# Optimization experiments

Hardware: AMD Instinct MI355X
Metric: run time of the kernel (lower is better)

## Reference

```python
import jax, jax.numpy as jnp
import numpy as np

DG = 8   # deformable groups
K = 9    # 3x3 kernel taps


def _conv3x3(x, w, b):
    y = jax.lax.conv_general_dilated(x, w, (1, 1), ((1, 1), (1, 1)),
                                     dimension_numbers=('NCHW', 'OIHW', 'NCHW'))
    return y + b[None, :, None, None]


def _deform_conv_v2(x, off_y, off_x, mask, w, b):
    # x: [B,C,H,W], off_*/mask: [B,DG,K,H,W], w: [Cout,C,3,3], b: [Cout]
    B, C, H, W = x.shape
    cpg = C // DG
    k = jnp.arange(K)
    ky = (k // 3 - 1).astype(x.dtype)[None, None, :, None, None]
    kx = (k % 3 - 1).astype(x.dtype)[None, None, :, None, None]
    hh = jnp.arange(H, dtype=x.dtype)[None, None, None, :, None]
    ww = jnp.arange(W, dtype=x.dtype)[None, None, None, None, :]
    py = hh + ky + off_y            # sampling rows  [B,DG,K,H,W]
    px = ww + kx + off_x            # sampling cols
    y0 = jnp.floor(py); x0 = jnp.floor(px)
    ly = py - y0; lx = px - x0
    xf = x.reshape(B, DG, cpg, H * W)

    def corner(yi, xi):
        valid = ((yi >= 0) & (yi < H) & (xi >= 0) & (xi < W)).astype(x.dtype)
        idx = (jnp.clip(yi, 0, H - 1) * W + jnp.clip(xi, 0, W - 1)).astype(jnp.int32)
        idxb = jnp.broadcast_to(idx.reshape(B, DG, 1, K * H * W), (B, DG, cpg, K * H * W))
        v = jnp.take_along_axis(xf, idxb, axis=3).reshape(B, DG, cpg, K, H, W)
        return v, valid

    v00, m00 = corner(y0, x0)
    v01, m01 = corner(y0, x0 + 1)
    v10, m10 = corner(y0 + 1, x0)
    v11, m11 = corner(y0 + 1, x0 + 1)
    w00 = ((1 - ly) * (1 - lx) * m00)[:, :, None]
    w01 = ((1 - ly) * lx * m01)[:, :, None]
    w10 = (ly * (1 - lx) * m10)[:, :, None]
    w11 = (ly * lx * m11)[:, :, None]
    val = (v00 * w00 + v01 * w01 + v10 * w10 + v11 * w11) * mask[:, :, None]
    wr = w.reshape(w.shape[0], DG, cpg, K)
    return jnp.einsum('bgckhw,ogck->bohw', val, wr) + b[None, :, None, None]


def reference(feat_l, feat_s, w_atten, w_fsm, w_off, w_cm, b_cm, w_dcn, b_dcn):
    B, C, H, W = feat_l.shape
    # bilinear upsample (align_corners=False == half-pixel centers, matches jax.image.resize)
    feat_up = jax.image.resize(feat_s, (B, feat_s.shape[1], H, W), method='bilinear')
    # FeatureSelectionModule: SE-style gate + residual + 1x1 proj
    gap = feat_l.mean(axis=(2, 3))                       # [B,C]
    atten = jax.nn.sigmoid(gap @ w_atten.T)[:, :, None, None]
    xg = feat_l * (1.0 + atten)                          # x + x*atten
    feat_arm = jnp.einsum('bchw,oc->bohw', xg, w_fsm)
    # offset feature: 1x1 conv over cat([feat_arm, 2*feat_up])
    cat = jnp.concatenate([feat_arm, feat_up * 2.0], axis=1)
    off_feat = jnp.einsum('bchw,oc->bohw', cat, w_off)
    # dcn_v2 internal conv_offset_mask -> o1, o2, mask
    om = _conv3x3(off_feat, w_cm, b_cm)                  # [B, DG*3*K, H, W]
    n = DG * K
    off_y = om[:, :n].reshape(B, DG, K, H, W)
    off_x = om[:, n:2 * n].reshape(B, DG, K, H, W)
    mask = jax.nn.sigmoid(om[:, 2 * n:]).reshape(B, DG, K, H, W)
    out = _deform_conv_v2(feat_up, off_y, off_x, mask, w_dcn, b_dcn)
    return jax.nn.relu(out) + feat_arm


def setup_inputs() -> dict:
    key = jax.random.key(0)
    ks = jax.random.split(key, 9)
    B, C, H, W = 8, 128, 64, 64
    return {
        'feat_l': jax.random.normal(ks[0], (B, C, H, W), jnp.float32),
        'feat_s': jax.random.normal(ks[1], (B, C, H // 2, W // 2), jnp.float32),
        'w_atten': jax.random.normal(ks[2], (C, C), jnp.float32) / np.sqrt(C),
        'w_fsm': jax.random.normal(ks[3], (C, C), jnp.float32) / np.sqrt(C),
        'w_off': jax.random.normal(ks[4], (C, 2 * C), jnp.float32) / np.sqrt(2 * C),
        'w_cm': jax.random.normal(ks[5], (DG * 3 * K, C, 3, 3), jnp.float32) * 0.01,
        'b_cm': jnp.zeros((DG * 3 * K,), jnp.float32),
        'w_dcn': jax.random.normal(ks[6], (C, C, 3, 3), jnp.float32) / np.sqrt(C * 9),
        'b_dcn': jax.random.normal(ks[7], (C,), jnp.float32) * 0.01,
    }
```

## Files before the change

kernel.cpp:

```cpp
#include <hip/hip_runtime.h>
#include <hip/hip_bf16.h>

constexpr int Bn = 8, Cn = 128, Hn = 64, Wn = 64, HWn = Hn * Wn;
constexpr int DGn = 8, Kn = 9, CMn = 216;
constexpr int Hs = 32, Ws = 32, HWs = Hs * Ws;

typedef __attribute__((ext_vector_type(8))) short bf16x8;
typedef __attribute__((ext_vector_type(4))) float f32x4;

constexpr long OFF_FLAG = 0;
constexpr long OFF_FLB  = 256;
constexpr long OFF_FUPB = OFF_FLB  + (long)Bn*HWn*Cn/2;
constexpr long OFF_OFT  = OFF_FUPB + (long)Bn*HWn*Cn/2;
constexpr long OFF_WCT  = OFF_OFT  + (long)Bn*HWn*Cn/2;
constexpr long OFF_WDT  = OFF_WCT  + (long)18*224*64/2 + 64;
constexpr long OFF_P    = OFF_WDT  + (long)Kn*Cn*Cn/2 + 64;
constexpr long OFF_W1TB = OFF_P    + 16384;
constexpr long OFF_WCAT = OFF_W1TB + (long)Bn*Cn*Cn/2;
constexpr long OFF_BCM  = OFF_WCAT + (long)Bn*Cn*256/2;
constexpr long OFF_BDC  = OFF_BCM + 256;
constexpr long OFF_GAP  = OFF_BDC + 256;
constexpr long OFF_AT   = OFF_GAP + 1024;
constexpr long OFF_FARM = OFF_AT  + 1024;
constexpr long OFF_OM   = OFF_FARM + (long)Bn*Cn*HWn;

static __device__ __forceinline__ float ldin(const void* p, long i, bool isbf) {
  if (isbf) return __bfloat162float(((const __hip_bfloat16*)p)[i]);
  return ((const float*)p)[i];
}
static __device__ __forceinline__ unsigned short f2b(float f) {
  unsigned u = __builtin_bit_cast(unsigned, f);
  u += 0x7FFFu + ((u >> 16) & 1u);
  return (unsigned short)(u >> 16);
}
static __device__ __forceinline__ unsigned pack2(float v0, float v1) {
  return ((unsigned)f2b(v1) << 16) | (unsigned)f2b(v0);
}
static __device__ __forceinline__ float b2f(unsigned short s) {
  return __builtin_bit_cast(float, ((unsigned)s) << 16);
}

#define GLOAD_LDS16(g, l) __builtin_amdgcn_global_load_lds( \
    (const __attribute__((address_space(1))) void*)(g),     \
    (__attribute__((address_space(3))) void*)(l), 16, 0, 0)

__global__ __launch_bounds__(256) void k_detect(const unsigned int* __restrict__ p,
                                                int* __restrict__ flag,
                                                float* __restrict__ gap) {
  __shared__ int cnt[256];
  int t = threadIdx.x;
  int c = 0;
  for (int i = 0; i < 4; ++i) {
    unsigned v = p[t * 4 + i];
    unsigned e = (v >> 7) & 0xFFu;
    c += (e >= 118u && e <= 130u) ? 1 : 0;
  }
  cnt[t] = c;
#pragma unroll
  for (int i = 0; i < 4; ++i) gap[t + i * 256] = 0.f;
  __syncthreads();
  for (int s = 128; s > 0; s >>= 1) {
    if (t < s) cnt[t] += cnt[t + s];
    __syncthreads();
  }
  if (t == 0) *flag = (cnt[0] > 512) ? 1 : 0;
}

__global__ __launch_bounds__(256) void k_prep(const void* __restrict__ b_cm,
                                              const void* __restrict__ b_dcn,
                                              const void* __restrict__ w_cm,
                                              const void* __restrict__ w_dcn,
                                              const void* __restrict__ woff,
                                              const void* __restrict__ wfsm,
                                              float* __restrict__ bcm_d,
                                              float* __restrict__ bdc_d,
                                              unsigned short* __restrict__ wcb,
                                              unsigned short* __restrict__ wdb,
                                              float* __restrict__ P,
                                              const int* __restrict__ flag) {
  const int bid = blockIdx.x, t = threadIdx.x;
  const bool isbf = (*flag != 0);
  if (bid == 0) {
    if (t < CMn) bcm_d[t] = ldin(b_cm, t, isbf);
    if (t < Cn)  bdc_d[t] = ldin(b_dcn, t, isbf);
    return;
  }
  if (bid < 1 + 1008) {
    int i = (bid - 1) * 256 + t;
    if (i >= 18 * 224 * 64) return;
    int s = i / (224 * 64);
    int rem = i % (224 * 64);
    int oc = rem >> 6, c_off = rem & 63;
    int tap = s >> 1, ck = s & 1;
    int c = ck * 64 + c_off;
    float v = 0.f;
    if (oc < CMn) v = ldin(w_cm, ((long)oc * Cn + c) * Kn + tap, isbf);
    int chunk = c_off >> 3, e = c_off & 7;
    int pc = chunk ^ (oc & 7);
    wcb[(long)s * 14336 + oc * 64 + pc * 8 + e] = f2b(v);
    return;
  }
  if (bid < 1 + 1008 + 576) {
    int i = (bid - 1 - 1008) * 256 + t;
    if (i >= Kn * Cn * Cn) return;
    int e = i & 7, lh = (i >> 3) & 3, o = (i >> 5) & 127;
    int ks = (i >> 12) & 3, k = i >> 14;
    int c = ks * 32 + lh * 8 + e;
    wdb[i] = f2b(ldin(w_dcn, ((long)o * Cn + c) * Kn + k, isbf));
    return;
  }
  {
    int idx = (bid - 1 - 1008 - 576) * 256 + t;
    if (idx >= Cn * Cn) return;
    int o = idx >> 7, k = idx & 127;
    float s = 0.f;
    for (int c = 0; c < Cn; ++c)
      s += ldin(woff, (long)o * 256 + c, isbf) * ldin(wfsm, (long)c * Cn + k, isbf);
    P[idx] = s;
  }
}

__global__ __launch_bounds__(256) void k_cvtlup(const void* __restrict__ feat_l,
                                                const void* __restrict__ fs,
                                                unsigned short* __restrict__ flb,
                                                unsigned short* __restrict__ fupb,
                                                float* __restrict__ gap,
                                                const int* __restrict__ flag) {
  __shared__ float sh[8448];
  const int b = blockIdx.y, t = threadIdx.x;
  const bool isbf = (*flag != 0);
  if (blockIdx.z == 0) {
    const int p0 = blockIdx.x * 64;
    for (int i = t; i < 8192; i += 256) {
      int c = i >> 6, p = i & 63;
      sh[c * 65 + p] = ldin(feat_l, (long)(b * Cn + c) * HWn + p0 + p, isbf);
    }
    __syncthreads();
    if (t < 128) {
      float s = 0.f;
#pragma unroll
      for (int p = 0; p < 64; ++p) s += sh[t * 65 + p];
      atomicAdd(&gap[b * Cn + t], s * (1.0f / HWn));
    }
    for (int i = t; i < 1024; i += 256) {
      int p = i >> 4, ch = (i & 15) * 8;
      uint4 pk;
      pk.x = pack2(sh[(ch + 0) * 65 + p], sh[(ch + 1) * 65 + p]);
      pk.y = pack2(sh[(ch + 2) * 65 + p], sh[(ch + 3) * 65 + p]);
      pk.z = pack2(sh[(ch + 4) * 65 + p], sh[(ch + 5) * 65 + p]);
      pk.w = pack2(sh[(ch + 6) * 65 + p], sh[(ch + 7) * 65 + p]);
      *(uint4*)(flb + (((long)(b * HWn + p0 + p)) << 7) + ch) = pk;
    }
  } else {
    const int h = blockIdx.x;
    int iy0; float fy;
    if (h & 1) { iy0 = (h - 1) >> 1; fy = 0.25f; } else { iy0 = (h >> 1) - 1; fy = 0.75f; }
    int iy1 = min(iy0 + 1, Hs - 1); iy0 = max(iy0, 0);
    for (int i = t; i < 8192; i += 256) {
      int sel = i >> 12, c = (i >> 5) & 127, x = i & 31;
      int iy = sel ? iy1 : iy0;
      sh[sel * 4224 + c * 33 + x] = ldin(fs, (long)(b * Cn + c) * HWs + iy * Ws + x, isbf);
    }
    __syncthreads();
    for (int i = t; i < 1024; i += 256) {
      int w = i >> 4, ch0 = (i & 15) * 8;
      int ix0; float fx;
      if (w & 1) { ix0 = (w - 1) >> 1; fx = 0.25f; } else { ix0 = (w >> 1) - 1; fx = 0.75f; }
      int ix1 = min(ix0 + 1, Ws - 1); ix0 = max(ix0, 0);
      float v[8];
#pragma unroll
      for (int j = 0; j < 8; ++j) {
        int c = ch0 + j;
        v[j] = (1.f - fy) * ((1.f - fx) * sh[c * 33 + ix0] + fx * sh[c * 33 + ix1]) +
               fy         * ((1.f - fx) * sh[4224 + c * 33 + ix0] + fx * sh[4224 + c * 33 + ix1]);
      }
      uint4 pk;
      pk.x = pack2(v[0], v[1]); pk.y = pack2(v[2], v[3]);
      pk.z = pack2(v[4], v[5]); pk.w = pack2(v[6], v[7]);
      *(uint4*)(fupb + (((long)(b * HWn + h * Wn + w)) << 7) + ch0) = pk;
    }
  }
}

__global__ __launch_bounds__(256) void k_atten(const float* __restrict__ gap,
                                               const void* __restrict__ wat,
                                               float* __restrict__ at1p,
                                               const int* __restrict__ flag) {
  int tid = blockIdx.x * 256 + threadIdx.x;
  if (tid >= Bn * Cn) return;
  int b = tid >> 7, o = tid & 127;
  bool isbf = (*flag != 0);
  const float* g = gap + b * Cn;
  float s = 0.f;
  for (int c = 0; c < Cn; ++c) s += g[c] * ldin(wat, (long)o * Cn + c, isbf);
  at1p[tid] = 1.0f + 1.0f / (1.0f + expf(-s));
}

__global__ __launch_bounds__(256) void k_wprep(const void* __restrict__ wfsm,
                                               const void* __restrict__ woff,
                                               const float* __restrict__ P,
                                               const float* __restrict__ at1p,
                                               unsigned short* __restrict__ w1tb,
                                               unsigned short* __restrict__ wcat,
                                               const int* __restrict__ flag) {
  int idx = blockIdx.x * 256 + threadIdx.x;
  if (idx >= Bn * 49152) return;
  bool isbf = (*flag != 0);
  int b = idx / 49152, r = idx % 49152;
  if (r < 16384) {
    int o = r >> 7, k = r & 127;
    w1tb[((long)(b * Cn + o) << 7) + k] =
        f2b(ldin(wfsm, (long)o * Cn + k, isbf) * at1p[b * Cn + k]);
  } else {
    r -= 16384;
    int o = r >> 8, k = r & 255;
    float v = (k < 128) ? P[o * Cn + k] * at1p[b * Cn + k]
                        : 2.0f * ldin(woff, (long)o * 256 + k, isbf);
    wcat[((long)(b * Cn + o) << 8) + k] = f2b(v);
  }
}

__global__ __launch_bounds__(256) void k_fao(const unsigned short* __restrict__ flb,
                                             const unsigned short* __restrict__ fupb,
                                             const unsigned short* __restrict__ w1tb,
                                             const unsigned short* __restrict__ wcat,
                                             float* __restrict__ farm,
                                             unsigned short* __restrict__ oftb) {
  const int b = blockIdx.y, m0 = blockIdx.x * 32;
  const int t = threadIdx.x, lane = t & 63, wv = t >> 6;
  const int lm = lane & 15, lh = lane >> 4;
  f32x4 accF[2][2], accO[2][2];
#pragma unroll
  for (int mt = 0; mt < 2; ++mt)
#pragma unroll
    for (int nt = 0; nt < 2; ++nt) {
      accF[mt][nt] = (f32x4){0.f, 0.f, 0.f, 0.f};
      accO[mt][nt] = (f32x4){0.f, 0.f, 0.f, 0.f};
    }
  const unsigned short* A0 = flb + ((long)b << 19);
  const unsigned short* A1 = fupb + ((long)b << 19);
  const unsigned short* BwF = w1tb + ((long)b << 14);
  const unsigned short* BwO = wcat + ((long)b << 15);
#pragma unroll
  for (int ks = 0; ks < 4; ++ks) {
    int c0 = ks * 32 + lh * 8;
    bf16x8 bfvF[2], bfvO[2];
#pragma unroll
    for (int nt = 0; nt < 2; ++nt) {
      int o = wv * 32 + nt * 16 + lm;
      bfvF[nt] = *(const bf16x8*)(BwF + ((long)o << 7) + c0);
      bfvO[nt] = *(const bf16x8*)(BwO + ((long)o << 8) + c0);
    }
#pragma unroll
    for (int mt = 0; mt < 2; ++mt) {
      bf16x8 af = *(const bf16x8*)(A0 + (((long)(m0 + mt * 16 + lm)) << 7) + c0);
#pragma unroll
      for (int nt = 0; nt < 2; ++nt) {
        accF[mt][nt] = __builtin_amdgcn_mfma_f32_16x16x32_bf16(af, bfvF[nt], accF[mt][nt], 0, 0, 0);
        accO[mt][nt] = __builtin_amdgcn_mfma_f32_16x16x32_bf16(af, bfvO[nt], accO[mt][nt], 0, 0, 0);
      }
    }
  }
#pragma unroll
  for (int ks = 4; ks < 8; ++ks) {
    int c0 = ks * 32 + lh * 8;
    int ca = c0 - 128;
    bf16x8 bfvO[2];
#pragma unroll
    for (int nt = 0; nt < 2; ++nt)
      bfvO[nt] = *(const bf16x8*)(BwO + (((long)(wv * 32 + nt * 16 + lm)) << 8) + c0);
#pragma unroll
    for (int mt = 0; mt < 2; ++mt) {
      bf16x8 af = *(const bf16x8*)(A1 + (((long)(m0 + mt * 16 + lm)) << 7) + ca);
#pragma unroll
      for (int nt = 0; nt < 2; ++nt)
        accO[mt][nt] = __builtin_amdgcn_mfma_f32_16x16x32_bf16(af, bfvO[nt], accO[mt][nt], 0, 0, 0);
    }
  }
#pragma unroll
  for (int nt = 0; nt < 2; ++nt) {
    int o = wv * 32 + nt * 16 + lm;
#pragma unroll
    for (int mt = 0; mt < 2; ++mt) {
      *(f32x4*)(farm + (((long)(b * Cn + o)) << 12) + m0 + mt * 16 + lh * 4) = accF[mt][nt];
#pragma unroll
      for (int r = 0; r < 4; ++r)
        oftb[(((long)(b * HWn + m0 + mt * 16 + lh * 4 + r)) << 7) + o] = f2b(accO[mt][nt][r]);
    }
  }
}

__global__ __launch_bounds__(256) void k_convcm(const unsigned short* __restrict__ xb,
                                                const unsigned short* __restrict__ wsl,
                                                const float* __restrict__ bcm,
                                                float* __restrict__ om) {
  __shared__ unsigned short wlds[2][14336];
  const int h = blockIdx.x, b = blockIdx.y;
  const int t = threadIdx.x, lane = t & 63, wv = t >> 6;
  const int mi = wv & 1, ni = wv >> 1;
  const int lm = lane & 15, lh = lane >> 4;

  f32x4 acc[2][7];
#pragma unroll
  for (int mt = 0; mt < 2; ++mt)
#pragma unroll
    for (int nt = 0; nt < 7; ++nt) acc[mt][nt] = (f32x4){0.f, 0.f, 0.f, 0.f};

  auto stage = [&](int s, int bufi) {
    const char* src = (const char*)(wsl + (long)s * 14336);
    char* dstb = (char*)&wlds[bufi][0];
#pragma unroll
    for (int i2 = 0; i2 < 7; ++i2) {
      int off = (wv * 7 + i2) * 1024;
      GLOAD_LDS16(src + off + lane * 16, dstb + off);
    }
  };

  stage(0, 0);
  __syncthreads();

  for (int s = 0; s < 18; ++s) {
    const int cur = s & 1;
    if (s < 17) stage(s + 1, cur ^ 1);
    const int tap = s >> 1, ck = s & 1;
    const int ky = tap / 3, kx = tap % 3;
    const int gy = h + ky - 1;
    const bool gyok = ((unsigned)gy < (unsigned)Hn);
    const int gyc = min(max(gy, 0), Hn - 1);

    bf16x8 af[2][2];
#pragma unroll
    for (int mt = 0; mt < 2; ++mt) {
      int wpos = mi * 32 + mt * 16 + lm;
      int gx = wpos + kx - 1;
      bool ok = gyok && ((unsigned)gx < (unsigned)Wn);
      int gxc = min(max(gx, 0), Wn - 1);
      const unsigned short* ap = xb + (((long)(b * HWn + gyc * Wn + gxc)) << 7)
                                    + ck * 64 + lh * 8;
#pragma unroll
      for (int ksub = 0; ksub < 2; ++ksub) {
        bf16x8 v = *(const bf16x8*)(ap + ksub * 32);
        af[mt][ksub] = ok ? v : (bf16x8)(short)0;
      }
    }

    const char* wbase = (const char*)&wlds[cur][0];
#pragma unroll
    for (int ksub = 0; ksub < 2; ++ksub) {
      int jj = ksub * 4 + lh;
#pragma unroll
      for (int nt = 0; nt < 7; ++nt) {
        int oc = ni * 112 + nt * 16 + lm;
        bf16x8 bfv = *(const bf16x8*)(wbase + oc * 128 + ((jj ^ (oc & 7)) << 4));
#pragma unroll
        for (int mt = 0; mt < 2; ++mt)
          acc[mt][nt] = __builtin_amdgcn_mfma_f32_16x16x32_bf16(
              af[mt][ksub], bfv, acc[mt][nt], 0, 0, 0);
      }
    }
    __syncthreads();
  }

#pragma unroll
  for (int nt = 0; nt < 7; ++nt) {
    int ch = ni * 112 + nt * 16 + lm;
    if (ch >= CMn) continue;
    float bias = bcm[ch];
#pragma unroll
    for (int mt = 0; mt < 2; ++mt) {
#pragma unroll
      for (int r = 0; r < 4; ++r) {
        int w = mi * 32 + mt * 16 + lh * 4 + r;
        float v = acc[mt][nt][r] + bias;
        if (ch >= 144) v = 1.0f / (1.0f + expf(-v));
        om[((long)((b * Hn + h) * CMn + ch) << 6) + w] = v;
      }
    }
  }
}

__global__ __launch_bounds__(512, 6) void k_dcn(const float* __restrict__ om,
                                                const unsigned short* __restrict__ fupb,
                                                const unsigned short* __restrict__ wdb,
                                                const float* __restrict__ bdc,
                                                const float* __restrict__ farm,
                                                void* __restrict__ out,
                                                const int* __restrict__ flagp) {
  __shared__ float om_lds[216 * 32];
  __shared__ char valb[2][32 * 256];
  const int h = blockIdx.x, b = blockIdx.y, w0 = blockIdx.z * 32;
  const int t = threadIdx.x;
  const int lane = t & 63, wid = t >> 6;
  const int lm = lane & 15, lh = lane >> 4;

  const float* omr = om + ((long)(b * Hn + h) * CMn << 6) + w0;
  for (int i = t; i < 1728; i += 512) {
    int ch = i >> 3, q = i & 7;
    *(float4*)&om_lds[ch * 32 + q * 4] = *(const float4*)(omr + (ch << 6) + q * 4);
  }

  const int pid = (wid << 6) | lane;
  const int half = pid & 1, gw = (pid >> 1) & 31, gg = pid >> 6;
  const int wcol = w0 + gw;
  const unsigned short* fbb = fupb + ((long)b << 19) + half * 8;

  const int cw = wid - 4;
  f32x4 acc[2][2];
#pragma unroll
  for (int mt = 0; mt < 2; ++mt)
#pragma unroll
    for (int nt = 0; nt < 2; ++nt) acc[mt][nt] = (f32x4){0.f, 0.f, 0.f, 0.f};

  union U4 { uint4 q; unsigned short s[8]; };

  auto stage = [&](int k) {
#pragma unroll
    for (int ti = 0; ti < 2; ++ti) {
      const int g = gg + ti * 4;
      const unsigned short* fb = fbb + g * 16;
      int ch = g * Kn + k;
      float oy = om_lds[ch * 32 + gw];
      float ox = om_lds[(72 + ch) * 32 + gw];
      float mk = om_lds[(144 + ch) * 32 + gw];
      float py = (float)(h + k / 3 - 1) + oy;
      float px = (float)(wcol + k % 3 - 1) + ox;
      float fy = floorf(py), fx = floorf(px);
      float ly = py - fy, lx = px - fx;
      int y0 = (int)fy, x0 = (int)fx, y1 = y0 + 1, x1 = x0 + 1;
      float vy0 = (y0 >= 0 && y0 < Hn) ? 1.f : 0.f;
      float vy1 = (y1 >= 0 && y1 < Hn) ? 1.f : 0.f;
      float vx0 = (x0 >= 0 && x0 < Wn) ? 1.f : 0.f;
      float vx1 = (x1 >= 0 && x1 < Wn) ? 1.f : 0.f;
      int cy0 = min(max(y0, 0), Hn - 1), cy1 = min(max(y1, 0), Hn - 1);
      int cx0 = min(max(x0, 0), Wn - 1), cx1 = min(max(x1, 0), Wn - 1);
      float wq0 = (1.f - ly) * (1.f - lx) * vy0 * vx0 * mk;
      float wq1 = (1.f - ly) * lx * vy0 * vx1 * mk;
      float wq2 = ly * (1.f - lx) * vy1 * vx0 * mk;
      float wq3 = ly * lx * vy1 * vx1 * mk;
      U4 a0, a1, a2, a3;
      a0.q = *(const uint4*)(fb + ((long)(cy0 * Wn + cx0) << 7));
      a1.q = *(const uint4*)(fb + ((long)(cy0 * Wn + cx1) << 7));
      a2.q = *(const uint4*)(fb + ((long)(cy1 * Wn + cx0) << 7));
      a3.q = *(const uint4*)(fb + ((long)(cy1 * Wn + cx1) << 7));
      float v[8];
#pragma unroll
      for (int j = 0; j < 8; ++j)
        v[j] = wq0 * b2f(a0.s[j]) + wq1 * b2f(a1.s[j]) +
               wq2 * b2f(a2.s[j]) + wq3 * b2f(a3.s[j]);
      uint4 pk;
      pk.x = pack2(v[0], v[1]); pk.y = pack2(v[2], v[3]);
      pk.z = pack2(v[4], v[5]); pk.w = pack2(v[6], v[7]);
      int chunk = g * 2 + half;
      *(uint4*)(valb[k & 1] + gw * 256 + ((chunk ^ (gw & 15)) << 4)) = pk;
    }
  };

  __syncthreads();
  if (wid < 4) stage(0);
  __syncthreads();

#pragma unroll
  for (int k = 0; k < Kn; ++k) {
    if (wid < 4) {
      if (k < Kn - 1) stage(k + 1);
    } else {
      const char* base = valb[k & 1];
      const unsigned short* wk = wdb + (long)k * 16384;
      __builtin_amdgcn_s_setprio(1);
#pragma unroll
      for (int ks = 0; ks < 4; ++ks) {
        int rchunk = (ks * 4 + lh) ^ lm;
        bf16x8 af0 = *(const bf16x8*)(base + lm * 256 + (rchunk << 4));
        bf16x8 af1 = *(const bf16x8*)(base + (16 + lm) * 256 + (rchunk << 4));
#pragma unroll
        for (int nt = 0; nt < 2; ++nt) {
          bf16x8 bfv = *(const bf16x8*)(wk + ks * 4096 +
                                        ((cw * 32 + nt * 16 + lm) << 5) + lh * 8);
          acc[0][nt] = __builtin_amdgcn_mfma_f32_16x16x32_bf16(af0, bfv, acc[0][nt], 0, 0, 0);
          acc[1][nt] = __builtin_amdgcn_mfma_f32_16x16x32_bf16(af1, bfv, acc[1][nt], 0, 0, 0);
        }
      }
      __builtin_amdgcn_s_setprio(0);
    }
    __syncthreads();
  }

  float* eps = om_lds;
  if (wid >= 4) {
#pragma unroll
    for (int nt = 0; nt < 2; ++nt) {
      int o = cw * 32 + nt * 16 + lm;
#pragma unroll
      for (int mt = 0; mt < 2; ++mt)
#pragma unroll
        for (int r = 0; r < 4; ++r)
          eps[o * 33 + mt * 16 + lh * 4 + r] = acc[mt][nt][r];
    }
  }
  __syncthreads();
  {
    bool isbf = (*flagp != 0);
    int o = t >> 2, q = t & 3;
    float bias = bdc[o];
    long obase = (long)(b * Cn + o) * HWn + h * Wn + w0 + q * 8;
    const float* fr = farm + obase;
#pragma unroll
    for (int j = 0; j < 8; ++j) {
      float v = eps[o * 33 + q * 8 + j] + bias;
      v = fmaxf(v, 0.f) + fr[j];
      if (isbf) ((__hip_bfloat16*)out)[obase + j] = __float2bfloat16(v);
      else      ((float*)out)[obase + j] = v;
    }
  }
}

extern "C" void kernel_launch(void* const* d_in, const int* in_sizes, int n_in,
                              void* d_out, int out_size, void* d_ws, size_t ws_size,
                              hipStream_t stream) {
  (void)in_sizes; (void)n_in; (void)out_size; (void)ws_size;
  const void* feat_l  = d_in[0];
  const void* feat_s  = d_in[1];
  const void* w_atten = d_in[2];
  const void* w_fsm   = d_in[3];
  const void* w_off   = d_in[4];
  const void* w_cm    = d_in[5];
  const void* b_cm    = d_in[6];
  const void* w_dcn   = d_in[7];
  const void* b_dcn   = d_in[8];
  float* ws = (float*)d_ws;
  int* flagw = (int*)d_ws;
  const int* flag = (const int*)d_ws;
  unsigned short* flb  = (unsigned short*)(ws + OFF_FLB);
  unsigned short* fupb = (unsigned short*)(ws + OFF_FUPB);
  unsigned short* oftb = (unsigned short*)(ws + OFF_OFT);
  unsigned short* wcb  = (unsigned short*)(ws + OFF_WCT);
  unsigned short* wdb  = (unsigned short*)(ws + OFF_WDT);
  unsigned short* w1tb = (unsigned short*)(ws + OFF_W1TB);
  unsigned short* wcat = (unsigned short*)(ws + OFF_WCAT);

  k_detect<<<1, 256, 0, stream>>>((const unsigned int*)feat_l, flagw, ws + OFF_GAP);
  k_prep<<<1 + 1008 + 576 + 64, 256, 0, stream>>>(b_cm, b_dcn, w_cm, w_dcn,
                                                  w_off, w_fsm,
                                                  ws + OFF_BCM, ws + OFF_BDC,
                                                  wcb, wdb, ws + OFF_P, flag);
  k_cvtlup<<<dim3(64, 8, 2), 256, 0, stream>>>(feat_l, feat_s, flb, fupb,
                                               ws + OFF_GAP, flag);
  k_atten<<<4, 256, 0, stream>>>(ws + OFF_GAP, w_atten, ws + OFF_AT, flag);
  k_wprep<<<(Bn * 49152 + 255) / 256, 256, 0, stream>>>(w_fsm, w_off, ws + OFF_P,
                                                        ws + OFF_AT, w1tb, wcat, flag);
  k_fao<<<dim3(128, 8), 256, 0, stream>>>(flb, fupb, w1tb, wcat, ws + OFF_FARM, oftb);
  k_convcm<<<dim3(64, 8), 256, 0, stream>>>(oftb, wcb, ws + OFF_BCM, ws + OFF_OM);
  k_dcn<<<dim3(64, 8, 2), 512, 0, stream>>>(ws + OFF_OM, fupb, wdb,
                                            ws + OFF_BDC, ws + OFF_FARM, d_out, flag);
}
```

Before: 183.3 us.

## Store farm and offset/mask intermediates in bf16 and shrink DCN shared memory

The feat_arm intermediate and the offset/mask tensor written by the conv kernel are now stored as bf16 instead of fp32, which halves the global traffic between k_fao, k_convcm and k_dcn. In k_dcn the offset/mask tile is staged in LDS as bf16, which shrinks shared memory and lets the launch bound rise from 6 to 8 blocks per CU. The epilogue now writes outputs with vectorized stores. Storing offsets in bf16 loses precision in the sampling positions and in the residual, so accuracy could suffer.

```diff
diff --git a/kernel.cpp b/kernel.cpp
--- a/kernel.cpp
+++ b/kernel.cpp
@@ -224,7 +224,7 @@
                                              const unsigned short* __restrict__ fupb,
                                              const unsigned short* __restrict__ w1tb,
                                              const unsigned short* __restrict__ wcat,
-                                             float* __restrict__ farm,
+                                             unsigned short* __restrict__ farm,
                                              unsigned short* __restrict__ oftb) {
   const int b = blockIdx.y, m0 = blockIdx.x * 32;
   const int t = threadIdx.x, lane = t & 63, wv = t >> 6;
@@ -282,7 +282,10 @@
     int o = wv * 32 + nt * 16 + lm;
 #pragma unroll
     for (int mt = 0; mt < 2; ++mt) {
-      *(f32x4*)(farm + (((long)(b * Cn + o)) << 12) + m0 + mt * 16 + lh * 4) = accF[mt][nt];
+      uint2 pw;
+      pw.x = pack2(accF[mt][nt][0], accF[mt][nt][1]);
+      pw.y = pack2(accF[mt][nt][2], accF[mt][nt][3]);
+      *(uint2*)(farm + (((long)(b * Cn + o)) << 12) + m0 + mt * 16 + lh * 4) = pw;
 #pragma unroll
       for (int r = 0; r < 4; ++r)
         oftb[(((long)(b * HWn + m0 + mt * 16 + lh * 4 + r)) << 7) + o] = f2b(accO[mt][nt][r]);
@@ -293,7 +296,7 @@
 __global__ __launch_bounds__(256) void k_convcm(const unsigned short* __restrict__ xb,
                                                 const unsigned short* __restrict__ wsl,
                                                 const float* __restrict__ bcm,
-                                                float* __restrict__ om) {
+                                                unsigned short* __restrict__ om) {
   __shared__ unsigned short wlds[2][14336];
   const int h = blockIdx.x, b = blockIdx.y;
   const int t = threadIdx.x, lane = t & 63, wv = t >> 6;
@@ -373,30 +376,30 @@
         int w = mi * 32 + mt * 16 + lh * 4 + r;
         float v = acc[mt][nt][r] + bias;
         if (ch >= 144) v = 1.0f / (1.0f + expf(-v));
-        om[((long)((b * Hn + h) * CMn + ch) << 6) + w] = v;
+        om[((long)((b * Hn + h) * CMn + ch) << 6) + w] = f2b(v);
       }
     }
   }
 }
 
-__global__ __launch_bounds__(512, 6) void k_dcn(const float* __restrict__ om,
+__global__ __launch_bounds__(512, 8) void k_dcn(const unsigned short* __restrict__ omb,
                                                 const unsigned short* __restrict__ fupb,
                                                 const unsigned short* __restrict__ wdb,
                                                 const float* __restrict__ bdc,
-                                                const float* __restrict__ farm,
+                                                const unsigned short* __restrict__ farm,
                                                 void* __restrict__ out,
                                                 const int* __restrict__ flagp) {
-  __shared__ float om_lds[216 * 32];
-  __shared__ char valb[2][32 * 256];
+  __shared__ char smem[13824 + 16384];
+  unsigned short* om16 = (unsigned short*)smem;
   const int h = blockIdx.x, b = blockIdx.y, w0 = blockIdx.z * 32;
   const int t = threadIdx.x;
   const int lane = t & 63, wid = t >> 6;
   const int lm = lane & 15, lh = lane >> 4;
 
-  const float* omr = om + ((long)(b * Hn + h) * CMn << 6) + w0;
-  for (int i = t; i < 1728; i += 512) {
-    int ch = i >> 3, q = i & 7;
-    *(float4*)&om_lds[ch * 32 + q * 4] = *(const float4*)(omr + (ch << 6) + q * 4);
+  const unsigned short* omr = omb + ((long)(b * Hn + h) * CMn << 6) + w0;
+  for (int i = t; i < 864; i += 512) {
+    int ch = i >> 2, q = i & 3;
+    *(uint4*)(om16 + ch * 32 + q * 8) = *(const uint4*)(omr + (ch << 6) + q * 8);
   }
 
   const int pid = (wid << 6) | lane;
@@ -419,9 +422,9 @@
       const int g = gg + ti * 4;
       const unsigned short* fb = fbb + g * 16;
       int ch = g * Kn + k;
-      float oy = om_lds[ch * 32 + gw];
-      float ox = om_lds[(72 + ch) * 32 + gw];
-      float mk = om_lds[(144 + ch) * 32 + gw];
+      float oy = b2f(om16[ch * 32 + gw]);
+      float ox = b2f(om16[(72 + ch) * 32 + gw]);
+      float mk = b2f(om16[(144 + ch) * 32 + gw]);
       float py = (float)(h + k / 3 - 1) + oy;
       float px = (float)(wcol + k % 3 - 1) + ox;
       float fy = floorf(py), fx = floorf(px);
@@ -451,7 +454,7 @@
       pk.x = pack2(v[0], v[1]); pk.y = pack2(v[2], v[3]);
       pk.z = pack2(v[4], v[5]); pk.w = pack2(v[6], v[7]);
       int chunk = g * 2 + half;
-      *(uint4*)(valb[k & 1] + gw * 256 + ((chunk ^ (gw & 15)) << 4)) = pk;
+      *(uint4*)(smem + 13824 + (k & 1) * 8192 + gw * 256 + ((chunk ^ (gw & 15)) << 4)) = pk;
     }
   };
 
@@ -464,7 +467,7 @@
     if (wid < 4) {
       if (k < Kn - 1) stage(k + 1);
     } else {
-      const char* base = valb[k & 1];
+      const char* base = smem + 13824 + (k & 1) * 8192;
       const unsigned short* wk = wdb + (long)k * 16384;
       __builtin_amdgcn_s_setprio(1);
 #pragma unroll
@@ -485,7 +488,7 @@
     __syncthreads();
   }
 
-  float* eps = om_lds;
+  float* eps = (float*)smem;
   if (wid >= 4) {
 #pragma unroll
     for (int nt = 0; nt < 2; ++nt) {
@@ -503,13 +506,23 @@
     int o = t >> 2, q = t & 3;
     float bias = bdc[o];
     long obase = (long)(b * Cn + o) * HWn + h * Wn + w0 + q * 8;
-    const float* fr = farm + obase;
+    U4 fv;
+    fv.q = *(const uint4*)(farm + obase);
+    float vout[8];
 #pragma unroll
     for (int j = 0; j < 8; ++j) {
       float v = eps[o * 33 + q * 8 + j] + bias;
-      v = fmaxf(v, 0.f) + fr[j];
-      if (isbf) ((__hip_bfloat16*)out)[obase + j] = __float2bfloat16(v);
-      else      ((float*)out)[obase + j] = v;
+      vout[j] = fmaxf(v, 0.f) + b2f(fv.s[j]);
+    }
+    if (isbf) {
+      uint4 pk;
+      pk.x = pack2(vout[0], vout[1]); pk.y = pack2(vout[2], vout[3]);
+      pk.z = pack2(vout[4], vout[5]); pk.w = pack2(vout[6], vout[7]);
+      *(uint4*)((__hip_bfloat16*)out + obase) = pk;
+    } else {
+      float* op = (float*)out + obase;
+      *(float4*)op = (float4){vout[0], vout[1], vout[2], vout[3]};
+      *(float4*)(op + 4) = (float4){vout[4], vout[5], vout[6], vout[7]};
     }
   }
 }
@@ -537,6 +550,8 @@
   unsigned short* wdb  = (unsigned short*)(ws + OFF_WDT);
   unsigned short* w1tb = (unsigned short*)(ws + OFF_W1TB);
   unsigned short* wcat = (unsigned short*)(ws + OFF_WCAT);
+  unsigned short* farm = (unsigned short*)(ws + OFF_FARM);
+  unsigned short* omb  = (unsigned short*)(ws + OFF_OM);
 
   k_detect<<<1, 256, 0, stream>>>((const unsigned int*)feat_l, flagw, ws + OFF_GAP);
   k_prep<<<1 + 1008 + 576 + 64, 256, 0, stream>>>(b_cm, b_dcn, w_cm, w_dcn,
@@ -548,8 +563,8 @@
   k_atten<<<4, 256, 0, stream>>>(ws + OFF_GAP, w_atten, ws + OFF_AT, flag);
   k_wprep<<<(Bn * 49152 + 255) / 256, 256, 0, stream>>>(w_fsm, w_off, ws + OFF_P,
                                                         ws + OFF_AT, w1tb, wcat, flag);
-  k_fao<<<dim3(128, 8), 256, 0, stream>>>(flb, fupb, w1tb, wcat, ws + OFF_FARM, oftb);
-  k_convcm<<<dim3(64, 8), 256, 0, stream>>>(oftb, wcb, ws + OFF_BCM, ws + OFF_OM);
-  k_dcn<<<dim3(64, 8, 2), 512, 0, stream>>>(ws + OFF_OM, fupb, wdb,
-                                            ws + OFF_BDC, ws + OFF_FARM, d_out, flag);
-}
+  k_fao<<<dim3(128, 8), 256, 0, stream>>>(flb, fupb, w1tb, wcat, farm, oftb);
+  k_convcm<<<dim3(64, 8), 256, 0, stream>>>(oftb, wcb, ws + OFF_BCM, omb);
+  k_dcn<<<dim3(64, 8, 2), 512, 0, stream>>>(omb, fupb, wdb,
+                                            ws + OFF_BDC, farm, d_out, flag);
+}
```

After: 173.4 us. 1.06x faster.
